# Kernel tuning notes

Hardware: AMD Instinct MI355X
Metric: run time of the kernel (lower is better)

The kernel has to match this reference:

```python
import jax, jax.numpy as jnp
import numpy as np

NEG_BIG = -9e15

def setup_inputs() -> dict:
    key = jax.random.key(0)
    k1, k2, k3, k4 = jax.random.split(key, 4)
    N, F_in, F_out = 8192, 512, 128
    return {
        "input": jax.random.normal(k1, (N, F_in), dtype=jnp.float32),
        "adj": jax.random.randint(k2, (N, N), 0, 2, dtype=jnp.int32),
        "W": jax.random.normal(k3, (F_in, F_out), dtype=jnp.float32) * 0.05,
        "a": jax.random.normal(k4, (2 * F_out, 1), dtype=jnp.float32) * 0.05,
    }

def reference(input, adj, W, a):
    alpha = 0.2  # LeakyReLU negative slope
    h = input @ W                      # [N, F_out]
    F_out = h.shape[1]
    # concat score decomposition: a^T [h_i || h_j] = h_i @ a1 + h_j @ a2
    a1 = a[:F_out, 0]                  # [F_out]
    a2 = a[F_out:, 0]                  # [F_out]
    e = jax.nn.leaky_relu(h @ a1[:, None] + (h @ a2)[None, :], negative_slope=alpha)  # [N, N]
    e = jnp.where(adj > 0, e, NEG_BIG)
    attention = jax.nn.softmax(e, axis=1)
    h_prime = attention @ h            # [N, F_out]
    return jax.nn.elu(h_prime)         # concat=True
```

## Files before the change

kernel.cpp:

```cpp
#include <hip/hip_runtime.h>
#include <hip/hip_bf16.h>


typedef __attribute__((ext_vector_type(4))) float f32x4;
typedef __attribute__((ext_vector_type(8))) short s16x8;

#define N_NODES 8192
#define F_IN 512
#define F_OUT 128
#define JS 8
#define JCHUNK (N_NODES / JS)

static __device__ __forceinline__ short f2bf(float f) {
  __hip_bfloat16 h = __float2bfloat16(f);
  return __builtin_bit_cast(short, h);
}

__global__ __launch_bounds__(256) void k_mask(const int* __restrict__ adj,
    unsigned long long* __restrict__ mask) {
  const int nwaves = gridDim.x * 4;
  int wid = blockIdx.x * 4 + (threadIdx.x >> 6);
  int lane = threadIdx.x & 63;
  const int ntasks = N_NODES * (N_NODES / 64);
  for (int task = wid; task < ntasks; task += nwaves) {
    int row = task >> 7;
    int cg = task & 127;
    int v = adj[(size_t)row * N_NODES + cg * 64 + lane];
    unsigned long long b = __ballot(v != 0);
    if (lane == 0) mask[(size_t)row * (N_NODES / 64) + cg] = b;
  }
}

__global__ void k0a_wt(const float* __restrict__ W, unsigned short* __restrict__ WT) {
  int idx = blockIdx.x * 256 + threadIdx.x;
  int k = idx >> 7, f = idx & 127;
  WT[(size_t)f * F_IN + k] = (unsigned short)f2bf(W[idx]);
}

__global__ void k0c_wa(const float* __restrict__ W, const float* __restrict__ a,
                       float* __restrict__ wa) {
  int k = blockIdx.x * 256 + threadIdx.x;
  if (k >= F_IN) return;
  const float* Wr = W + (size_t)k * F_OUT;
  float d1 = 0.f, d2 = 0.f;
#pragma unroll 8
  for (int f = 0; f < F_OUT; f += 4) {
    f32x4 w  = *(const f32x4*)(Wr + f);
    f32x4 a1 = *(const f32x4*)(a + f);
    f32x4 a2 = *(const f32x4*)(a + F_OUT + f);
    d1 += w[0] * a1[0] + w[1] * a1[1] + w[2] * a1[2] + w[3] * a1[3];
    d2 += w[0] * a2[0] + w[1] * a2[1] + w[2] * a2[2] + w[3] * a2[3];
  }
  wa[k] = d1;
  wa[F_IN + k] = d2;
}

__global__ __launch_bounds__(256) void k0b_x(const float* __restrict__ X,
    const float* __restrict__ wa, unsigned short* __restrict__ Xb,
    f32x4* __restrict__ rowdat, unsigned* __restrict__ pE) {
  int wave = threadIdx.x >> 6, lane = threadIdx.x & 63;
  int i = blockIdx.x * 4 + wave;
  const float* Xr = X + (size_t)i * F_IN + lane * 8;
  f32x4 x0 = ((const f32x4*)Xr)[0];
  f32x4 x1 = ((const f32x4*)Xr)[1];
  f32x4 w10 = ((const f32x4*)(wa + lane * 8))[0];
  f32x4 w11 = ((const f32x4*)(wa + lane * 8))[1];
  f32x4 w20 = ((const f32x4*)(wa + F_IN + lane * 8))[0];
  f32x4 w21 = ((const f32x4*)(wa + F_IN + lane * 8))[1];

  s16x8 xb;
#pragma unroll
  for (int e = 0; e < 4; e++) { xb[e] = f2bf(x0[e]); xb[e + 4] = f2bf(x1[e]); }
  *(s16x8*)(Xb + (size_t)i * F_IN + lane * 8) = xb;

  float d1 = 0.f, d2 = 0.f;
#pragma unroll
  for (int e = 0; e < 4; e++) {
    d1 += x0[e] * w10[e] + x1[e] * w11[e];
    d2 += x0[e] * w20[e] + x1[e] * w21[e];
  }
#pragma unroll
  for (int m = 1; m < 64; m <<= 1) {
    d1 += __shfl_xor(d1, m, 64);
    d2 += __shfl_xor(d2, m, 64);
  }
  if (lane == 0) {
    float s1 = d1, s2 = d2;
    f32x4 rd;
    rd[0] = expf(s1);
    rd[1] = expf(0.2f * s1);
    rd[2] = expf(-s1);
    rd[3] = 0.f;
    rowdat[i] = rd;
    unsigned e2  = (unsigned)(unsigned short)f2bf(expf(s2));
    unsigned e2s = (unsigned)(unsigned short)f2bf(expf(0.2f * s2));
    pE[i] = (e2s << 16) | e2;
  }
}

__global__ __launch_bounds__(256) void k1_gemm(const unsigned short* __restrict__ WT,
    const unsigned short* __restrict__ Xb, unsigned short* __restrict__ hT) {
  int wave = threadIdx.x >> 6, lane = threadIdx.x & 63;
  int lrow = lane & 15, grp = lane >> 4;
  int tile = blockIdx.x * 4 + wave;
  int fb = tile & 7;
  int nb = tile >> 3;

  const unsigned short* Ar = WT + (size_t)(fb * 16 + lrow) * F_IN + grp * 8;
  const unsigned short* Br = Xb + (size_t)(nb * 16 + lrow) * F_IN + grp * 8;

  f32x4 acc = (f32x4)(0.0f);
#pragma unroll
  for (int k0 = 0; k0 < F_IN; k0 += 32) {
    s16x8 af = *(const s16x8*)(Ar + k0);
    s16x8 bf = *(const s16x8*)(Br + k0);
    acc = __builtin_amdgcn_mfma_f32_16x16x32_bf16(af, bf, acc, 0, 0, 0);
  }
#pragma unroll
  for (int r = 0; r < 4; r++)
    hT[(size_t)(fb * 16 + grp * 4 + r) * N_NODES + nb * 16 + lrow] =
        (unsigned short)f2bf(acc[r]);
}

__global__ __launch_bounds__(256, 4) void k2_main(const unsigned* __restrict__ mask32,
    const unsigned short* __restrict__ hT, const f32x4* __restrict__ rowdat,
    const unsigned* __restrict__ pE, float* __restrict__ accws,
    float* __restrict__ denws) {
  int js = blockIdx.x & (JS - 1);
  int rb = blockIdx.x / JS;
  int wave = threadIdx.x >> 6, lane = threadIdx.x & 63;
  int lrow = lane & 15, grp = lane >> 4;
  int waveRow = rb * 64 + wave * 16;
  int i0 = waveRow + lrow;
  int jlo = js * JCHUNK;

  f32x4 rd = rowdat[i0];
  float E1 = rd[0], E1s = rd[1], T1 = rd[2];

  f32x4 acc[8];
#pragma unroll
  for (int n = 0; n < 8; n++) acc[n] = (f32x4)(0.0f);
  float dsum = 0.f;

#define PROC(pe, e)                                                  \
  {                                                                  \
    unsigned pu = (pe);                                              \
    float E2  = __builtin_bit_cast(float, pu << 16);                 \
    float E2s = __builtin_bit_cast(float, pu & 0xffff0000u);         \
    float sel = (E2 > T1) ? E1 * E2 : E1s * E2s;                     \
    float p = ((b >> e) & 1u) ? sel : 0.f;                           \
    dsum += p;                                                       \
    af[e] = f2bf(p);                                                 \
  }

  for (int sc = 0; sc < JCHUNK / 512; sc++) {
    int jbase = jlo + sc * 512;
    const uint4* mrow =
        (const uint4*)(mask32 + (size_t)i0 * (N_NODES / 32) + jbase / 32);
    uint4 mm[4];
#pragma unroll
    for (int c = 0; c < 4; c++) mm[c] = mrow[c];

#pragma unroll
    for (int t = 0; t < 16; t++) {
      int jj = jbase + t * 32 + grp * 8;
      unsigned b = (mm[t >> 2][t & 3] >> (grp * 8)) & 0xffu;
      const uint4* pp = (const uint4*)(pE + jj);
      uint4 P0 = pp[0], P1 = pp[1];
      s16x8 af;
      PROC(P0.x, 0); PROC(P0.y, 1); PROC(P0.z, 2); PROC(P0.w, 3);
      PROC(P1.x, 4); PROC(P1.y, 5); PROC(P1.z, 6); PROC(P1.w, 7);
      const unsigned short* hTj = hT + jj;
#pragma unroll
      for (int n = 0; n < 8; n++) {
        s16x8 bf = *(const s16x8*)(hTj + (size_t)(n * 16 + lrow) * N_NODES);
        acc[n] = __builtin_amdgcn_mfma_f32_16x16x32_bf16(af, bf, acc[n], 0, 0, 0);
      }
    }
  }
#undef PROC

  dsum += __shfl_xor(dsum, 16, 64);
  dsum += __shfl_xor(dsum, 32, 64);
  if (lane < 16) denws[js * N_NODES + waveRow + lane] = dsum;

#pragma unroll
  for (int n = 0; n < 8; n++)
#pragma unroll
    for (int r = 0; r < 4; r++)
      accws[((size_t)js * N_NODES + waveRow + grp * 4 + r) * F_OUT + n * 16 + lrow] =
          acc[n][r];
}

__global__ void k3_fin(const float* __restrict__ accws,
                       const float* __restrict__ denws, float* __restrict__ out) {
  int idx4 = blockIdx.x * 256 + threadIdx.x;
  int i = idx4 >> 5;
  const int S4 = N_NODES * F_OUT / 4;
  f32x4 s = (f32x4)(0.0f);
  float d = 0.f;
#pragma unroll
  for (int js = 0; js < JS; js++) {
    s += ((const f32x4*)accws)[idx4 + js * S4];
    d += denws[i + js * N_NODES];
  }
  f32x4 v = s / d;
#pragma unroll
  for (int e = 0; e < 4; e++) v[e] = v[e] > 0.f ? v[e] : expm1f(v[e]);
  ((f32x4*)out)[idx4] = v;
}

extern "C" void kernel_launch(void* const* d_in, const int* in_sizes, int n_in,
                              void* d_out, int out_size, void* d_ws, size_t ws_size,
                              hipStream_t stream) {
  const float* X   = (const float*)d_in[0];
  const int*   adj = (const int*)d_in[1];
  const float* W   = (const float*)d_in[2];
  const float* a   = (const float*)d_in[3];
  float* out = (float*)d_out;

  char* ws = (char*)d_ws;
  size_t off = 0;
  unsigned short* WT = (unsigned short*)(ws + off); off += (size_t)F_OUT * F_IN * 2;
  unsigned short* Xb = (unsigned short*)(ws + off); off += (size_t)N_NODES * F_IN * 2;
  unsigned short* hT = (unsigned short*)(ws + off); off += (size_t)F_OUT * N_NODES * 2;
  f32x4* rowdat = (f32x4*)(ws + off); off += (size_t)N_NODES * 16;
  unsigned* pE = (unsigned*)(ws + off); off += (size_t)N_NODES * 4;
  float* wa = (float*)(ws + off); off += (size_t)2 * F_IN * 4;
  unsigned long long* mask = (unsigned long long*)(ws + off);
  off += (size_t)N_NODES * (N_NODES / 64) * 8;
  float* accws = (float*)(ws + off); off += (size_t)JS * N_NODES * F_OUT * 4;
  float* denws = (float*)(ws + off); off += (size_t)JS * N_NODES * 4;
  (void)in_sizes; (void)n_in; (void)out_size; (void)ws_size;

  k_mask<<<2048, 256, 0, stream>>>(adj, mask);
  k0a_wt<<<(F_IN * F_OUT) / 256, 256, 0, stream>>>(W, WT);
  k0c_wa<<<2, 256, 0, stream>>>(W, a, wa);
  k0b_x<<<N_NODES / 4, 256, 0, stream>>>(X, wa, Xb, rowdat, pE);
  k1_gemm<<<1024, 256, 0, stream>>>(WT, Xb, hT);
  k2_main<<<(N_NODES / 64) * JS, 256, 0, stream>>>((const unsigned*)mask, hT,
                                                   rowdat, pE, accws, denws);
  k3_fin<<<(N_NODES * F_OUT) / 4 / 256, 256, 0, stream>>>(accws, denws, out);
}
```

Before: 552.1 us.

## Fuse mask, GEMM and finalize into fewer kernels reading adj directly

```diff
diff --git a/kernel.cpp b/kernel.cpp
--- a/kernel.cpp
+++ b/kernel.cpp
@@ -8,206 +8,217 @@
 #define N_NODES 8192
 #define F_IN 512
 #define F_OUT 128
-#define JS 8
-#define JCHUNK (N_NODES / JS)
+#define CHUNK 256
+#define NCHUNK (N_NODES / CHUNK)
+#define PSTRIDE 272
 
 static __device__ __forceinline__ short f2bf(float f) {
   __hip_bfloat16 h = __float2bfloat16(f);
   return __builtin_bit_cast(short, h);
 }
 
-__global__ __launch_bounds__(256) void k_mask(const int* __restrict__ adj,
-    unsigned long long* __restrict__ mask) {
-  const int nwaves = gridDim.x * 4;
-  int wid = blockIdx.x * 4 + (threadIdx.x >> 6);
-  int lane = threadIdx.x & 63;
-  const int ntasks = N_NODES * (N_NODES / 64);
-  for (int task = wid; task < ntasks; task += nwaves) {
-    int row = task >> 7;
-    int cg = task & 127;
-    int v = adj[(size_t)row * N_NODES + cg * 64 + lane];
-    unsigned long long b = __ballot(v != 0);
-    if (lane == 0) mask[(size_t)row * (N_NODES / 64) + cg] = b;
-  }
-}
-
-__global__ void k0a_wt(const float* __restrict__ W, unsigned short* __restrict__ WT) {
-  int idx = blockIdx.x * 256 + threadIdx.x;
-  int k = idx >> 7, f = idx & 127;
-  WT[(size_t)f * F_IN + k] = (unsigned short)f2bf(W[idx]);
-}
-
-__global__ void k0c_wa(const float* __restrict__ W, const float* __restrict__ a,
-                       float* __restrict__ wa) {
-  int k = blockIdx.x * 256 + threadIdx.x;
-  if (k >= F_IN) return;
-  const float* Wr = W + (size_t)k * F_OUT;
-  float d1 = 0.f, d2 = 0.f;
+__global__ __launch_bounds__(256) void kA(const float* __restrict__ W,
+    const float* __restrict__ a, unsigned short* __restrict__ WT,
+    float* __restrict__ wa) {
+  int b = blockIdx.x;
+  if (b < 256) {
+    int idx = b * 256 + threadIdx.x;
+    int k = idx >> 7, f = idx & 127;
+    WT[(size_t)f * F_IN + k] = (unsigned short)f2bf(W[idx]);
+  } else {
+    int k = (b - 256) * 256 + threadIdx.x;
+    if (k < F_IN) {
+      const float* Wr = W + (size_t)k * F_OUT;
+      float d1 = 0.f, d2 = 0.f;
 #pragma unroll 8
-  for (int f = 0; f < F_OUT; f += 4) {
-    f32x4 w  = *(const f32x4*)(Wr + f);
-    f32x4 a1 = *(const f32x4*)(a + f);
-    f32x4 a2 = *(const f32x4*)(a + F_OUT + f);
-    d1 += w[0] * a1[0] + w[1] * a1[1] + w[2] * a1[2] + w[3] * a1[3];
-    d2 += w[0] * a2[0] + w[1] * a2[1] + w[2] * a2[2] + w[3] * a2[3];
-  }
-  wa[k] = d1;
-  wa[F_IN + k] = d2;
-}
-
-__global__ __launch_bounds__(256) void k0b_x(const float* __restrict__ X,
-    const float* __restrict__ wa, unsigned short* __restrict__ Xb,
-    f32x4* __restrict__ rowdat, unsigned* __restrict__ pE) {
+      for (int f = 0; f < F_OUT; f += 4) {
+        f32x4 w  = *(const f32x4*)(Wr + f);
+        f32x4 a1 = *(const f32x4*)(a + f);
+        f32x4 a2 = *(const f32x4*)(a + F_OUT + f);
+        d1 += w[0] * a1[0] + w[1] * a1[1] + w[2] * a1[2] + w[3] * a1[3];
+        d2 += w[0] * a2[0] + w[1] * a2[1] + w[2] * a2[2] + w[3] * a2[3];
+      }
+      wa[k] = d1;
+      wa[F_IN + k] = d2;
+    }
+  }
+}
+
+__global__ __launch_bounds__(256) void kStage(const float* __restrict__ X,
+    const float* __restrict__ wa, const unsigned short* __restrict__ WT,
+    f32x4* __restrict__ rowdat, unsigned* __restrict__ pE,
+    unsigned short* __restrict__ hT) {
+  int b = blockIdx.x;
   int wave = threadIdx.x >> 6, lane = threadIdx.x & 63;
-  int i = blockIdx.x * 4 + wave;
-  const float* Xr = X + (size_t)i * F_IN + lane * 8;
-  f32x4 x0 = ((const f32x4*)Xr)[0];
-  f32x4 x1 = ((const f32x4*)Xr)[1];
-  f32x4 w10 = ((const f32x4*)(wa + lane * 8))[0];
-  f32x4 w11 = ((const f32x4*)(wa + lane * 8))[1];
-  f32x4 w20 = ((const f32x4*)(wa + F_IN + lane * 8))[0];
-  f32x4 w21 = ((const f32x4*)(wa + F_IN + lane * 8))[1];
-
-  s16x8 xb;
-#pragma unroll
-  for (int e = 0; e < 4; e++) { xb[e] = f2bf(x0[e]); xb[e + 4] = f2bf(x1[e]); }
-  *(s16x8*)(Xb + (size_t)i * F_IN + lane * 8) = xb;
-
-  float d1 = 0.f, d2 = 0.f;
-#pragma unroll
-  for (int e = 0; e < 4; e++) {
-    d1 += x0[e] * w10[e] + x1[e] * w11[e];
-    d2 += x0[e] * w20[e] + x1[e] * w21[e];
-  }
-#pragma unroll
-  for (int m = 1; m < 64; m <<= 1) {
-    d1 += __shfl_xor(d1, m, 64);
-    d2 += __shfl_xor(d2, m, 64);
-  }
-  if (lane == 0) {
-    float s1 = d1, s2 = d2;
-    f32x4 rd;
-    rd[0] = expf(s1);
-    rd[1] = expf(0.2f * s1);
-    rd[2] = expf(-s1);
-    rd[3] = 0.f;
-    rowdat[i] = rd;
-    unsigned e2  = (unsigned)(unsigned short)f2bf(expf(s2));
-    unsigned e2s = (unsigned)(unsigned short)f2bf(expf(0.2f * s2));
-    pE[i] = (e2s << 16) | e2;
-  }
-}
-
-__global__ __launch_bounds__(256) void k1_gemm(const unsigned short* __restrict__ WT,
-    const unsigned short* __restrict__ Xb, unsigned short* __restrict__ hT) {
+
+  if (b < 1024) {
+    int lrow = lane & 15, grp = lane >> 4;
+    int tile = b * 4 + wave;
+    int fb = tile & 7;
+    int nb = tile >> 3;
+    const unsigned short* Ar = WT + (size_t)(fb * 16 + lrow) * F_IN + grp * 8;
+    const float* Br = X + (size_t)(nb * 16 + lrow) * F_IN + grp * 8;
+
+    f32x4 acc = (f32x4)(0.0f);
+#pragma unroll
+    for (int k0 = 0; k0 < F_IN; k0 += 32) {
+      s16x8 af = *(const s16x8*)(Ar + k0);
+      f32x4 b0 = *(const f32x4*)(Br + k0);
+      f32x4 b1 = *(const f32x4*)(Br + k0 + 4);
+      s16x8 bf;
+#pragma unroll
+      for (int e = 0; e < 4; e++) { bf[e] = f2bf(b0[e]); bf[e + 4] = f2bf(b1[e]); }
+      acc = __builtin_amdgcn_mfma_f32_16x16x32_bf16(af, bf, acc, 0, 0, 0);
+    }
+#pragma unroll
+    for (int r = 0; r < 4; r++)
+      hT[(size_t)(fb * 16 + grp * 4 + r) * N_NODES + nb * 16 + lrow] =
+          (unsigned short)f2bf(acc[r]);
+  } else {
+    int i = (b - 1024) * 4 + wave;
+    const float* Xr = X + (size_t)i * F_IN + lane * 8;
+    f32x4 x0 = ((const f32x4*)Xr)[0];
+    f32x4 x1 = ((const f32x4*)Xr)[1];
+    f32x4 w10 = ((const f32x4*)(wa + lane * 8))[0];
+    f32x4 w11 = ((const f32x4*)(wa + lane * 8))[1];
+    f32x4 w20 = ((const f32x4*)(wa + F_IN + lane * 8))[0];
+    f32x4 w21 = ((const f32x4*)(wa + F_IN + lane * 8))[1];
+    float d1 = 0.f, d2 = 0.f;
+#pragma unroll
+    for (int e = 0; e < 4; e++) {
+      d1 += x0[e] * w10[e] + x1[e] * w11[e];
+      d2 += x0[e] * w20[e] + x1[e] * w21[e];
+    }
+#pragma unroll
+    for (int m = 1; m < 64; m <<= 1) {
+      d1 += __shfl_xor(d1, m, 64);
+      d2 += __shfl_xor(d2, m, 64);
+    }
+    if (lane == 0) {
+      float s1 = d1, s2 = d2;
+      f32x4 rd;
+      rd[0] = expf(s1);
+      rd[1] = expf(0.2f * s1);
+      rd[2] = expf(-s1);
+      rd[3] = 0.f;
+      rowdat[i] = rd;
+      unsigned e2  = (unsigned)(unsigned short)f2bf(expf(s2));
+      unsigned e2s = (unsigned)(unsigned short)f2bf(expf(0.2f * s2));
+      pE[i] = (e2s << 16) | e2;
+    }
+  }
+}
+
+__global__ __launch_bounds__(256, 2) void kMain(const int* __restrict__ adj,
+    const unsigned short* __restrict__ hT, const f32x4* __restrict__ rowdat,
+    const unsigned* __restrict__ pE, float* __restrict__ out) {
+  __shared__ unsigned short P_lds[16 * PSTRIDE];
+  __shared__ float sden[16];
+
   int wave = threadIdx.x >> 6, lane = threadIdx.x & 63;
   int lrow = lane & 15, grp = lane >> 4;
-  int tile = blockIdx.x * 4 + wave;
-  int fb = tile & 7;
-  int nb = tile >> 3;
-
-  const unsigned short* Ar = WT + (size_t)(fb * 16 + lrow) * F_IN + grp * 8;
-  const unsigned short* Br = Xb + (size_t)(nb * 16 + lrow) * F_IN + grp * 8;
-
-  f32x4 acc = (f32x4)(0.0f);
-#pragma unroll
-  for (int k0 = 0; k0 < F_IN; k0 += 32) {
-    s16x8 af = *(const s16x8*)(Ar + k0);
-    s16x8 bf = *(const s16x8*)(Br + k0);
-    acc = __builtin_amdgcn_mfma_f32_16x16x32_bf16(af, bf, acc, 0, 0, 0);
-  }
-#pragma unroll
-  for (int r = 0; r < 4; r++)
-    hT[(size_t)(fb * 16 + grp * 4 + r) * N_NODES + nb * 16 + lrow] =
-        (unsigned short)f2bf(acc[r]);
-}
-
-__global__ __launch_bounds__(256, 4) void k2_main(const unsigned* __restrict__ mask32,
-    const unsigned short* __restrict__ hT, const f32x4* __restrict__ rowdat,
-    const unsigned* __restrict__ pE, float* __restrict__ accws,
-    float* __restrict__ denws) {
-  int js = blockIdx.x & (JS - 1);
-  int rb = blockIdx.x / JS;
-  int wave = threadIdx.x >> 6, lane = threadIdx.x & 63;
-  int lrow = lane & 15, grp = lane >> 4;
-  int waveRow = rb * 64 + wave * 16;
-  int i0 = waveRow + lrow;
-  int jlo = js * JCHUNK;
-
-  f32x4 rd = rowdat[i0];
-  float E1 = rd[0], E1s = rd[1], T1 = rd[2];
-
-  f32x4 acc[8];
-#pragma unroll
-  for (int n = 0; n < 8; n++) acc[n] = (f32x4)(0.0f);
-  float dsum = 0.f;
-
-#define PROC(pe, e)                                                  \
-  {                                                                  \
-    unsigned pu = (pe);                                              \
-    float E2  = __builtin_bit_cast(float, pu << 16);                 \
-    float E2s = __builtin_bit_cast(float, pu & 0xffff0000u);         \
-    float sel = (E2 > T1) ? E1 * E2 : E1s * E2s;                     \
-    float p = ((b >> e) & 1u) ? sel : 0.f;                           \
-    dsum += p;                                                       \
-    af[e] = f2bf(p);                                                 \
-  }
-
-  for (int sc = 0; sc < JCHUNK / 512; sc++) {
-    int jbase = jlo + sc * 512;
-    const uint4* mrow =
-        (const uint4*)(mask32 + (size_t)i0 * (N_NODES / 32) + jbase / 32);
-    uint4 mm[4];
-#pragma unroll
-    for (int c = 0; c < 4; c++) mm[c] = mrow[c];
-
-#pragma unroll
-    for (int t = 0; t < 16; t++) {
-      int jj = jbase + t * 32 + grp * 8;
-      unsigned b = (mm[t >> 2][t & 3] >> (grp * 8)) & 0xffu;
-      const uint4* pp = (const uint4*)(pE + jj);
-      uint4 P0 = pp[0], P1 = pp[1];
-      s16x8 af;
-      PROC(P0.x, 0); PROC(P0.y, 1); PROC(P0.z, 2); PROC(P0.w, 3);
-      PROC(P1.x, 4); PROC(P1.y, 5); PROC(P1.z, 6); PROC(P1.w, 7);
-      const unsigned short* hTj = hT + jj;
-#pragma unroll
-      for (int n = 0; n < 8; n++) {
-        s16x8 bf = *(const s16x8*)(hTj + (size_t)(n * 16 + lrow) * N_NODES);
-        acc[n] = __builtin_amdgcn_mfma_f32_16x16x32_bf16(af, bf, acc[n], 0, 0, 0);
-      }
-    }
-  }
-#undef PROC
-
-  dsum += __shfl_xor(dsum, 16, 64);
-  dsum += __shfl_xor(dsum, 32, 64);
-  if (lane < 16) denws[js * N_NODES + waveRow + lane] = dsum;
-
-#pragma unroll
-  for (int n = 0; n < 8; n++)
-#pragma unroll
-    for (int r = 0; r < 4; r++)
-      accws[((size_t)js * N_NODES + waveRow + grp * 4 + r) * F_OUT + n * 16 + lrow] =
-          acc[n][r];
-}
-
-__global__ void k3_fin(const float* __restrict__ accws,
-                       const float* __restrict__ denws, float* __restrict__ out) {
-  int idx4 = blockIdx.x * 256 + threadIdx.x;
-  int i = idx4 >> 5;
-  const int S4 = N_NODES * F_OUT / 4;
-  f32x4 s = (f32x4)(0.0f);
-  float d = 0.f;
-#pragma unroll
-  for (int js = 0; js < JS; js++) {
-    s += ((const f32x4*)accws)[idx4 + js * S4];
-    d += denws[i + js * N_NODES];
-  }
-  f32x4 v = s / d;
-#pragma unroll
-  for (int e = 0; e < 4; e++) v[e] = v[e] > 0.f ? v[e] : expm1f(v[e]);
-  ((f32x4*)out)[idx4] = v;
+  int rbase = blockIdx.x * 16;
+
+  float E1[4], E1s[4], T1[4];
+#pragma unroll
+  for (int rr = 0; rr < 4; rr++) {
+    f32x4 rd = rowdat[rbase + wave * 4 + rr];
+    E1[rr] = rd[0]; E1s[rr] = rd[1]; T1[rr] = rd[2];
+  }
+
+  const int* adjbase = adj + (size_t)(rbase + wave * 4) * N_NODES + lane * 4;
+  const unsigned* pEl = pE + lane * 4;
+
+  float dsum[4] = {0.f, 0.f, 0.f, 0.f};
+  f32x4 acc[2];
+  acc[0] = (f32x4)(0.0f);
+  acc[1] = (f32x4)(0.0f);
+
+#define PROC1(av, pv, rr, pout)                                   \
+  {                                                               \
+    unsigned pu = (pv);                                           \
+    float E2  = __builtin_bit_cast(float, pu << 16);              \
+    float E2s = __builtin_bit_cast(float, pu & 0xffff0000u);      \
+    float sel = (E2 > T1[rr]) ? E1[rr] * E2 : E1s[rr] * E2s;      \
+    pout = ((av) != 0) ? sel : 0.f;                               \
+    dsum[rr] += pout;                                             \
+  }
+
+#define PROCPACK(A4, P4, rr, lo, hi)                              \
+  {                                                               \
+    float p0, p1, p2, p3;                                         \
+    PROC1(A4.x, P4.x, rr, p0) PROC1(A4.y, P4.y, rr, p1)           \
+    PROC1(A4.z, P4.z, rr, p2) PROC1(A4.w, P4.w, rr, p3)           \
+    lo = ((unsigned)(unsigned short)f2bf(p1) << 16) |             \
+         (unsigned)(unsigned short)f2bf(p0);                      \
+    hi = ((unsigned)(unsigned short)f2bf(p3) << 16) |             \
+         (unsigned)(unsigned short)f2bf(p2);                      \
+  }
+
+#define BODY(USEA, USEP, PREA, PREP, C)                                        \
+  {                                                                            \
+    int cn = ((C) < NCHUNK - 1) ? (C) + 1 : 0;                                 \
+    _Pragma("unroll")                                                          \
+    for (int rr = 0; rr < 4; rr++)                                             \
+      PREA[rr] = *(const int4*)(adjbase + (size_t)rr * N_NODES + cn * CHUNK);  \
+    PREP = *(const uint4*)(pEl + cn * CHUNK);                                  \
+    _Pragma("unroll")                                                          \
+    for (int rr = 0; rr < 4; rr++) {                                           \
+      unsigned lo, hi;                                                         \
+      PROCPACK(USEA[rr], USEP, rr, lo, hi)                                     \
+      *(uint2*)((char*)P_lds + (wave * 4 + rr) * (PSTRIDE * 2) + lane * 8) =   \
+          make_uint2(lo, hi);                                                  \
+    }                                                                          \
+    __syncthreads();                                                           \
+    _Pragma("unroll")                                                          \
+    for (int t = 0; t < 8; t++) {                                              \
+      s16x8 af = *(const s16x8*)((const char*)P_lds + lrow * (PSTRIDE * 2) +   \
+                                 t * 64 + grp * 16);                           \
+      int jj = (C) * CHUNK + t * 32 + grp * 8;                                 \
+      _Pragma("unroll")                                                        \
+      for (int nt = 0; nt < 2; nt++) {                                         \
+        s16x8 bfv = *(const s16x8*)(hT +                                       \
+            (size_t)(wave * 32 + nt * 16 + lrow) * N_NODES + jj);              \
+        acc[nt] = __builtin_amdgcn_mfma_f32_16x16x32_bf16(af, bfv, acc[nt],    \
+                                                          0, 0, 0);            \
+      }                                                                        \
+    }                                                                          \
+    __syncthreads();                                                           \
+  }
+
+  int4 bufA[4], bufB[4];
+  uint4 bufPA, bufPB;
+#pragma unroll
+  for (int rr = 0; rr < 4; rr++)
+    bufA[rr] = *(const int4*)(adjbase + (size_t)rr * N_NODES);
+  bufPA = *(const uint4*)(pEl);
+
+  for (int cc = 0; cc < NCHUNK; cc += 2) {
+    BODY(bufA, bufPA, bufB, bufPB, cc)
+    BODY(bufB, bufPB, bufA, bufPA, cc + 1)
+  }
+#undef BODY
+#undef PROCPACK
+#undef PROC1
+
+#pragma unroll
+  for (int rr = 0; rr < 4; rr++) {
+    float d = dsum[rr];
+#pragma unroll
+    for (int m = 1; m < 64; m <<= 1) d += __shfl_xor(d, m, 64);
+    if (lane == 0) sden[wave * 4 + rr] = d;
+  }
+  __syncthreads();
+
+#pragma unroll
+  for (int nt = 0; nt < 2; nt++)
+#pragma unroll
+    for (int r = 0; r < 4; r++) {
+      int row = grp * 4 + r;
+      float v = acc[nt][r] / sden[row];
+      v = v > 0.f ? v : expm1f(v);
+      out[(size_t)(rbase + row) * F_OUT + wave * 32 + nt * 16 + lrow] = v;
+    }
 }
 
 extern "C" void kernel_launch(void* const* d_in, const int* in_sizes, int n_in,
@@ -222,23 +233,13 @@
   char* ws = (char*)d_ws;
   size_t off = 0;
   unsigned short* WT = (unsigned short*)(ws + off); off += (size_t)F_OUT * F_IN * 2;
-  unsigned short* Xb = (unsigned short*)(ws + off); off += (size_t)N_NODES * F_IN * 2;
   unsigned short* hT = (unsigned short*)(ws + off); off += (size_t)F_OUT * N_NODES * 2;
   f32x4* rowdat = (f32x4*)(ws + off); off += (size_t)N_NODES * 16;
   unsigned* pE = (unsigned*)(ws + off); off += (size_t)N_NODES * 4;
   float* wa = (float*)(ws + off); off += (size_t)2 * F_IN * 4;
-  unsigned long long* mask = (unsigned long long*)(ws + off);
-  off += (size_t)N_NODES * (N_NODES / 64) * 8;
-  float* accws = (float*)(ws + off); off += (size_t)JS * N_NODES * F_OUT * 4;
-  float* denws = (float*)(ws + off); off += (size_t)JS * N_NODES * 4;
   (void)in_sizes; (void)n_in; (void)out_size; (void)ws_size;
 
-  k_mask<<<2048, 256, 0, stream>>>(adj, mask);
-  k0a_wt<<<(F_IN * F_OUT) / 256, 256, 0, stream>>>(W, WT);
-  k0c_wa<<<2, 256, 0, stream>>>(W, a, wa);
-  k0b_x<<<N_NODES / 4, 256, 0, stream>>>(X, wa, Xb, rowdat, pE);
-  k1_gemm<<<1024, 256, 0, stream>>>(WT, Xb, hT);
-  k2_main<<<(N_NODES / 64) * JS, 256, 0, stream>>>((const unsigned*)mask, hT,
-                                                   rowdat, pE, accws, denws);
-  k3_fin<<<(N_NODES * F_OUT) / 4 / 256, 256, 0, stream>>>(accws, denws, out);
-}
+  kA<<<258, 256, 0, stream>>>(W, a, WT, wa);
+  kStage<<<3072, 256, 0, stream>>>(X, wa, WT, rowdat, pE, hT);
+  kMain<<<N_NODES / 16, 256, 0, stream>>>(adj, hT, rowdat, pE, out);
+}
```

Result: faster. 518.5 us (-6.1%).
